# Kernel tuning notes

Measured on AMD Instinct MI355X. Metric: run time of the kernel, lower is better.

The kernel has to match this reference:

```python
import jax, jax.numpy as jnp
import numpy as np

SEQ_LEN = 4096
DIM_HALF = 2048  # x last dim = 2 * DIM_HALF
DIM_OUT = 1024
LN_EPS = 1e-5


def setup_inputs() -> dict:
    key = jax.random.key(0)
    k1, k2, k3 = jax.random.split(key, 3)
    x = jax.random.normal(k1, (SEQ_LEN, 2 * DIM_HALF), dtype=jnp.float32)
    ln_scale = jnp.ones((DIM_HALF,), dtype=jnp.float32)
    # original init is uniform(-eps/n, eps/n); scale randn similarly small
    spatial_weights = jax.random.normal(k2, (SEQ_LEN, SEQ_LEN), dtype=jnp.float32) * (0.001 / SEQ_LEN)
    spatial_biases = jnp.ones((SEQ_LEN, 1), dtype=jnp.float32)
    proj_w = jax.random.normal(k3, (DIM_HALF, DIM_OUT), dtype=jnp.float32) * (1.0 / np.sqrt(DIM_HALF))
    proj_b = jnp.zeros((DIM_OUT,), dtype=jnp.float32)
    return {"x": x, "ln_scale": ln_scale, "spatial_weights": spatial_weights,
            "spatial_biases": spatial_biases, "proj_w": proj_w, "proj_b": proj_b}


def reference(x, ln_scale, spatial_weights, spatial_biases, proj_w, proj_b):
    # split into value half and gate half
    xh, gate = jnp.split(x, 2, axis=-1)  # each (n, d)
    # LayerNorm (scale only, no offset), haiku default eps=1e-5
    mean = jnp.mean(gate, axis=-1, keepdims=True)
    var = jnp.var(gate, axis=-1, keepdims=True)
    gate = (gate - mean) * jax.lax.rsqrt(var + LN_EPS) * ln_scale
    # causal (lower-triangular) masked spatial mixing: out[m,d] = sum_n w[m,n] * gate[n,d]
    n = spatial_weights.shape[0]
    w = jnp.tril(spatial_weights)
    gate = jnp.einsum('nd,mn->md', gate, w) + spatial_biases  # (n, d)
    # gating multiply + output projection
    out = (xh * gate) @ proj_w + proj_b  # (n, dim_out)
    return out
```

## Files before the change

kernel.cpp:

```cpp
#include <hip/hip_runtime.h>
#include <cstdint>
#include <cstddef>

#define SEQ 4096
#define DH 2048
#define DOUT 1024

typedef float f32x4 __attribute__((ext_vector_type(4)));
typedef __bf16 bf16x8 __attribute__((ext_vector_type(8)));


__device__ __forceinline__ unsigned short f2bf(float f) {
  unsigned int u = __float_as_uint(f);
  unsigned int r = (u + 0x7FFFu + ((u >> 16) & 1u)) >> 16;
  return (unsigned short)r;
}

__device__ __forceinline__ void g2l16(const unsigned short* g, unsigned short* l) {
  __builtin_amdgcn_global_load_lds((__attribute__((address_space(1))) void*)(void*)g,
                                   (__attribute__((address_space(3))) void*)l, 16, 0, 0);
}


__global__ __launch_bounds__(256) void ln_stats(const float* __restrict__ x,
                                                float* __restrict__ mv,
                                                float* __restrict__ rv) {
  int row = blockIdx.x;
  const float4* g4 = (const float4*)(x + (size_t)row * (2 * DH) + DH);
  float4 a = g4[threadIdx.x];
  float4 b = g4[threadIdx.x + 256];
  float s  = a.x + a.y + a.z + a.w + b.x + b.y + b.z + b.w;
  float s2 = a.x * a.x + a.y * a.y + a.z * a.z + a.w * a.w +
             b.x * b.x + b.y * b.y + b.z * b.z + b.w * b.w;
#pragma unroll
  for (int o = 32; o > 0; o >>= 1) {
    s  += __shfl_down(s, o);
    s2 += __shfl_down(s2, o);
  }
  __shared__ float red[8];
  int wave = threadIdx.x >> 6;
  if ((threadIdx.x & 63) == 0) { red[wave] = s; red[wave + 4] = s2; }
  __syncthreads();
  if (threadIdx.x == 0) {
    float S  = red[0] + red[1] + red[2] + red[3];
    float S2 = red[4] + red[5] + red[6] + red[7];
    float mean = S * (1.0f / DH);
    float var  = S2 * (1.0f / DH) - mean * mean;
    mv[row] = mean;
    rv[row] = rsqrtf(var + 1e-5f);
  }
}


__global__ __launch_bounds__(256) void norm_tr(const float* __restrict__ x,
                                               const float* __restrict__ mv,
                                               const float* __restrict__ rv,
                                               const float* __restrict__ lns,
                                               unsigned short* __restrict__ gateT) {
  __shared__ float tile[64][65];
  int d0 = blockIdx.x * 64;
  int n0 = blockIdx.y * 64;
#pragma unroll
  for (int i = 0; i < 16; i++) {
    int idx = threadIdx.x + i * 256;
    int r = idx >> 6, c = idx & 63;
    float v = x[(size_t)(n0 + r) * (2 * DH) + DH + d0 + c];
    tile[r][c] = (v - mv[n0 + r]) * rv[n0 + r];
  }
  __syncthreads();
#pragma unroll
  for (int i = 0; i < 16; i++) {
    int idx = threadIdx.x + i * 256;
    int dr = idx >> 6, nc = idx & 63;
    float v = tile[nc][dr] * lns[d0 + dr];
    gateT[(size_t)(d0 + dr) * SEQ + n0 + nc] = f2bf(v);
  }
}


__global__ __launch_bounds__(256) void cast_w_tril(const float* __restrict__ w,
                                                   unsigned short* __restrict__ wb) {
  size_t e = ((size_t)blockIdx.x * 256 + threadIdx.x) * 8;
  int m = (int)(e >> 12);
  int k = (int)(e & 4095);
  uint4 o;
  if (k + 7 <= m) {
    const float4* s = (const float4*)(w + e);
    float4 a = s[0], b = s[1];
    o.x = (unsigned)f2bf(a.x) | ((unsigned)f2bf(a.y) << 16);
    o.y = (unsigned)f2bf(a.z) | ((unsigned)f2bf(a.w) << 16);
    o.z = (unsigned)f2bf(b.x) | ((unsigned)f2bf(b.y) << 16);
    o.w = (unsigned)f2bf(b.z) | ((unsigned)f2bf(b.w) << 16);
  } else if (k > m) {
    o.x = o.y = o.z = o.w = 0u;
  } else {
    unsigned short t[8];
#pragma unroll
    for (int j = 0; j < 8; j++) t[j] = (k + j <= m) ? f2bf(w[e + j]) : (unsigned short)0;
    o.x = (unsigned)t[0] | ((unsigned)t[1] << 16);
    o.y = (unsigned)t[2] | ((unsigned)t[3] << 16);
    o.z = (unsigned)t[4] | ((unsigned)t[5] << 16);
    o.w = (unsigned)t[6] | ((unsigned)t[7] << 16);
  }
  *(uint4*)(wb + e) = o;
}


__global__ __launch_bounds__(256) void proj_tr(const float* __restrict__ pw,
                                               unsigned short* __restrict__ pT) {
  __shared__ float tile[64][65];
  int j0 = blockIdx.x * 64;
  int d0 = blockIdx.y * 64;
#pragma unroll
  for (int i = 0; i < 16; i++) {
    int idx = threadIdx.x + i * 256;
    int r = idx >> 6, c = idx & 63;
    tile[r][c] = pw[(size_t)(d0 + r) * DOUT + j0 + c];
  }
  __syncthreads();
#pragma unroll
  for (int i = 0; i < 16; i++) {
    int idx = threadIdx.x + i * 256;
    int jr = idx >> 6, dc = idx & 63;
    pT[(size_t)(j0 + jr) * DH + d0 + dc] = f2bf(tile[dc][jr]);
  }
}


template <int BM, int BN, int EPI, bool CAUSAL>
__global__ __launch_bounds__(256) void gemm_t(const unsigned short* __restrict__ A,
                                              const unsigned short* __restrict__ BT,
                                              const float* __restrict__ xfull,
                                              const float* __restrict__ rbias,
                                              unsigned short* __restrict__ Pout,
                                              const float* __restrict__ cbias,
                                              float* __restrict__ out,
                                              int N, int K) {
  constexpr int BK = 64;
  constexpr int MI = BM / 32;
  constexpr int NJ = BN / 32;
  constexpr int ARPT = (BM * BK) / (256 * 8);
  constexpr int BRPT = (BN * BK) / (256 * 8);

  __shared__ unsigned short sA[BM * BK];
  __shared__ unsigned short sB[BN * BK];

  const int tid = threadIdx.x;
  const int lane = tid & 63, wave = tid >> 6;
  const int quad = lane >> 4, l16 = lane & 15;
  const int wm = wave >> 1, wn = wave & 1;
  const int bn0 = blockIdx.x * BN;

  int by = blockIdx.y;
  if (CAUSAL) {
    int q = by >> 4, r = by & 15;
    by = (q == 0) ? r : (q == 1) ? (31 - r) : (q == 2) ? (32 + r) : (63 - r);
  }
  const int bm0 = by * BM;
  const int kEnd = CAUSAL ? (bm0 + BM) : K;

  const unsigned short* aSrc[ARPT];
  unsigned short* aDst[ARPT];
  const unsigned short* bSrc[BRPT];
  unsigned short* bDst[BRPT];
#pragma unroll
  for (int r = 0; r < ARPT; r++) {
    int idx = r * 256 + tid;
    int row = idx >> 3;
    int col = ((idx & 7) ^ (row & 7)) * 8;
    aSrc[r] = A + (size_t)(bm0 + row) * K + col;
    aDst[r] = &sA[(size_t)idx * 8];
  }
#pragma unroll
  for (int r = 0; r < BRPT; r++) {
    int idx = r * 256 + tid;
    int row = idx >> 3;
    int col = ((idx & 7) ^ (row & 7)) * 8;
    bSrc[r] = BT + (size_t)(bn0 + row) * K + col;
    bDst[r] = &sB[(size_t)idx * 8];
  }

  f32x4 acc[MI][NJ] = {};

  for (int k0 = 0; k0 < kEnd; k0 += BK) {
#pragma unroll
    for (int r = 0; r < ARPT; r++) { g2l16(aSrc[r], aDst[r]); aSrc[r] += BK; }
#pragma unroll
    for (int r = 0; r < BRPT; r++) { g2l16(bSrc[r], bDst[r]); bSrc[r] += BK; }
    __syncthreads();

    bf16x8 af[2][MI], bfr[2][NJ];
#pragma unroll
    for (int h = 0; h < 2; h++) {
#pragma unroll
      for (int i = 0; i < MI; i++) {
        int R = wm * (BM / 2) + i * 16 + l16;
        af[h][i] = *(const bf16x8*)&sA[R * BK + (((h * 4 + quad) ^ (R & 7)) * 8)];
      }
#pragma unroll
      for (int j = 0; j < NJ; j++) {
        int R = wn * (BN / 2) + j * 16 + l16;
        bfr[h][j] = *(const bf16x8*)&sB[R * BK + (((h * 4 + quad) ^ (R & 7)) * 8)];
      }
    }
#pragma unroll
    for (int h = 0; h < 2; h++)
#pragma unroll
      for (int i = 0; i < MI; i++)
#pragma unroll
        for (int j = 0; j < NJ; j++)
          acc[i][j] = __builtin_amdgcn_mfma_f32_16x16x32_bf16(af[h][i], bfr[h][j], acc[i][j], 0, 0, 0);
    __syncthreads();
  }

#pragma unroll
  for (int i = 0; i < MI; i++) {
#pragma unroll
    for (int j = 0; j < NJ; j++) {
      int col = bn0 + wn * (BN / 2) + j * 16 + l16;
#pragma unroll
      for (int r = 0; r < 4; r++) {
        int row = bm0 + wm * (BM / 2) + i * 16 + quad * 4 + r;
        float v = acc[i][j][r];
        if (EPI == 1) {
          float g = v + rbias[row];
          float pv = xfull[(size_t)row * (2 * DH) + col] * g;
          Pout[(size_t)row * N + col] = f2bf(pv);
        } else {
          out[(size_t)row * N + col] = v + cbias[col];
        }
      }
    }
  }
}


extern "C" void kernel_launch(void* const* d_in, const int* in_sizes, int n_in,
                              void* d_out, int out_size, void* d_ws, size_t ws_size,
                              hipStream_t stream) {
  (void)in_sizes; (void)n_in; (void)out_size; (void)ws_size;
  const float* x   = (const float*)d_in[0];
  const float* lns = (const float*)d_in[1];
  const float* w   = (const float*)d_in[2];
  const float* sb  = (const float*)d_in[3];
  const float* pw  = (const float*)d_in[4];
  const float* pb  = (const float*)d_in[5];
  float* out = (float*)d_out;

  char* p = (char*)d_ws;
  unsigned short* gateT = (unsigned short*)p; p += (size_t)DH * SEQ * 2;
  unsigned short* wb    = (unsigned short*)p; p += (size_t)SEQ * SEQ * 2;
  unsigned short* projT = (unsigned short*)p; p += (size_t)DOUT * DH * 2;
  unsigned short* Pbuf  = (unsigned short*)p; p += (size_t)SEQ * DH * 2;
  float* mv = (float*)p; p += (size_t)SEQ * 4;
  float* rv = (float*)p; p += (size_t)SEQ * 4;

  ln_stats<<<SEQ, 256, 0, stream>>>(x, mv, rv);
  norm_tr<<<dim3(DH / 64, SEQ / 64), 256, 0, stream>>>(x, mv, rv, lns, gateT);
  cast_w_tril<<<(int)(((size_t)SEQ * SEQ / 8) / 256), 256, 0, stream>>>(w, wb);
  proj_tr<<<dim3(DOUT / 64, DH / 64), 256, 0, stream>>>(pw, projT);

  gemm_t<64, 128, 1, true><<<dim3(DH / 128, SEQ / 64), 256, 0, stream>>>(
      wb, gateT, x, sb, Pbuf, nullptr, nullptr, DH, SEQ);
  gemm_t<64, 64, 2, false><<<dim3(DOUT / 64, SEQ / 64), 256, 0, stream>>>(
      Pbuf, projT, nullptr, nullptr, nullptr, pb, out, DOUT, DH);
}
```

Baseline: 267.1 us.

## Double-buffer LDS in GEMMs and pair causal row tiles for load balance

Rewrites the GEMM kernel to double-buffer its LDS tiles, issuing the global-to-LDS loads for the next K tile before computing the current one. This is meant to hide load latency and drops one barrier per iteration. The causal GEMM now gives each block a pair of row tiles (i and its mirror), so every block does the same amount of triangular work, replacing the old remapped block order. Tile shapes change to 128x64 for both GEMMs. LDS use doubles, which may lower occupancy, and the causal grid halves, giving fewer but longer blocks.

```diff
diff --git a/kernel.cpp b/kernel.cpp
--- a/kernel.cpp
+++ b/kernel.cpp
@@ -127,23 +127,24 @@
 }
 
 
-template <int BM, int BN, int EPI, bool CAUSAL>
-__global__ __launch_bounds__(256) void gemm_t(const unsigned short* __restrict__ A,
-                                              const unsigned short* __restrict__ BT,
-                                              const float* __restrict__ xfull,
-                                              const float* __restrict__ rbias,
-                                              unsigned short* __restrict__ Pout,
-                                              const float* __restrict__ cbias,
-                                              float* __restrict__ out,
-                                              int N, int K) {
+template <int BM, int BN, int EPI, bool PAIR>
+__global__ __launch_bounds__(256) void gemm_db(const unsigned short* __restrict__ A,
+                                               const unsigned short* __restrict__ BT,
+                                               const float* __restrict__ xfull,
+                                               const float* __restrict__ rbias,
+                                               unsigned short* __restrict__ Pout,
+                                               const float* __restrict__ cbias,
+                                               float* __restrict__ out,
+                                               int N, int K) {
   constexpr int BK = 64;
   constexpr int MI = BM / 32;
   constexpr int NJ = BN / 32;
   constexpr int ARPT = (BM * BK) / (256 * 8);
   constexpr int BRPT = (BN * BK) / (256 * 8);
-
-  __shared__ unsigned short sA[BM * BK];
-  __shared__ unsigned short sB[BN * BK];
+  constexpr int ASZ = BM * BK, BSZ = BN * BK;
+
+  __shared__ unsigned short sA[2 * ASZ];
+  __shared__ unsigned short sB[2 * BSZ];
 
   const int tid = threadIdx.x;
   const int lane = tid & 63, wave = tid >> 6;
@@ -151,83 +152,101 @@
   const int wm = wave >> 1, wn = wave & 1;
   const int bn0 = blockIdx.x * BN;
 
-  int by = blockIdx.y;
-  if (CAUSAL) {
-    int q = by >> 4, r = by & 15;
-    by = (q == 0) ? r : (q == 1) ? (31 - r) : (q == 2) ? (32 + r) : (63 - r);
-  }
-  const int bm0 = by * BM;
-  const int kEnd = CAUSAL ? (bm0 + BM) : K;
-
-  const unsigned short* aSrc[ARPT];
-  unsigned short* aDst[ARPT];
-  const unsigned short* bSrc[BRPT];
-  unsigned short* bDst[BRPT];
-#pragma unroll
-  for (int r = 0; r < ARPT; r++) {
-    int idx = r * 256 + tid;
-    int row = idx >> 3;
-    int col = ((idx & 7) ^ (row & 7)) * 8;
-    aSrc[r] = A + (size_t)(bm0 + row) * K + col;
-    aDst[r] = &sA[(size_t)idx * 8];
-  }
-#pragma unroll
-  for (int r = 0; r < BRPT; r++) {
-    int idx = r * 256 + tid;
-    int row = idx >> 3;
-    int col = ((idx & 7) ^ (row & 7)) * 8;
-    bSrc[r] = BT + (size_t)(bn0 + row) * K + col;
-    bDst[r] = &sB[(size_t)idx * 8];
-  }
-
-  f32x4 acc[MI][NJ] = {};
-
-  for (int k0 = 0; k0 < kEnd; k0 += BK) {
-#pragma unroll
-    for (int r = 0; r < ARPT; r++) { g2l16(aSrc[r], aDst[r]); aSrc[r] += BK; }
-#pragma unroll
-    for (int r = 0; r < BRPT; r++) { g2l16(bSrc[r], bDst[r]); bSrc[r] += BK; }
+  const int nPass = PAIR ? 2 : 1;
+  for (int pass = 0; pass < nPass; pass++) {
+    const int by = PAIR ? (pass == 0 ? (int)blockIdx.y
+                                     : (2 * (int)gridDim.y - 1 - (int)blockIdx.y))
+                        : (int)blockIdx.y;
+    const int bm0 = by * BM;
+    const int nt = (PAIR ? (bm0 + BM) : K) / BK;
+
+    const unsigned short* aP[ARPT];
+    const unsigned short* bP[BRPT];
+#pragma unroll
+    for (int r = 0; r < ARPT; r++) {
+      int idx = r * 256 + tid;
+      int row = idx >> 3;
+      int col = ((idx & 7) ^ (row & 7)) * 8;
+      aP[r] = A + (size_t)(bm0 + row) * K + col;
+    }
+#pragma unroll
+    for (int r = 0; r < BRPT; r++) {
+      int idx = r * 256 + tid;
+      int row = idx >> 3;
+      int col = ((idx & 7) ^ (row & 7)) * 8;
+      bP[r] = BT + (size_t)(bn0 + row) * K + col;
+    }
+
+    f32x4 acc[MI][NJ] = {};
+
+    auto stage = [&](int buf) {
+#pragma unroll
+      for (int r = 0; r < ARPT; r++) {
+        g2l16(aP[r], &sA[buf * ASZ + (r * 256 + tid) * 8]);
+        aP[r] += BK;
+      }
+#pragma unroll
+      for (int r = 0; r < BRPT; r++) {
+        g2l16(bP[r], &sB[buf * BSZ + (r * 256 + tid) * 8]);
+        bP[r] += BK;
+      }
+    };
+
+    auto compute = [&](int buf) {
+      const unsigned short* bA = &sA[buf * ASZ];
+      const unsigned short* bB = &sB[buf * BSZ];
+      bf16x8 af[2][MI], bfr[2][NJ];
+#pragma unroll
+      for (int h = 0; h < 2; h++) {
+#pragma unroll
+        for (int i = 0; i < MI; i++) {
+          int R = wm * (BM / 2) + i * 16 + l16;
+          af[h][i] = *(const bf16x8*)&bA[R * BK + (((h * 4 + quad) ^ (R & 7)) * 8)];
+        }
+#pragma unroll
+        for (int j = 0; j < NJ; j++) {
+          int R = wn * (BN / 2) + j * 16 + l16;
+          bfr[h][j] = *(const bf16x8*)&bB[R * BK + (((h * 4 + quad) ^ (R & 7)) * 8)];
+        }
+      }
+#pragma unroll
+      for (int h = 0; h < 2; h++)
+#pragma unroll
+        for (int i = 0; i < MI; i++)
+#pragma unroll
+          for (int j = 0; j < NJ; j++)
+            acc[i][j] = __builtin_amdgcn_mfma_f32_16x16x32_bf16(af[h][i], bfr[h][j], acc[i][j], 0, 0, 0);
+    };
+
+    if (pass) __syncthreads();
+    stage(0);
     __syncthreads();
 
-    bf16x8 af[2][MI], bfr[2][NJ];
-#pragma unroll
-    for (int h = 0; h < 2; h++) {
-#pragma unroll
-      for (int i = 0; i < MI; i++) {
-        int R = wm * (BM / 2) + i * 16 + l16;
-        af[h][i] = *(const bf16x8*)&sA[R * BK + (((h * 4 + quad) ^ (R & 7)) * 8)];
-      }
+    int cur = 0;
+    for (int t = 0; t < nt - 1; t++) {
+      stage(cur ^ 1);
+      compute(cur);
+      __syncthreads();
+      cur ^= 1;
+    }
+    compute(cur);
+
+#pragma unroll
+    for (int i = 0; i < MI; i++) {
 #pragma unroll
       for (int j = 0; j < NJ; j++) {
-        int R = wn * (BN / 2) + j * 16 + l16;
-        bfr[h][j] = *(const bf16x8*)&sB[R * BK + (((h * 4 + quad) ^ (R & 7)) * 8)];
-      }
-    }
-#pragma unroll
-    for (int h = 0; h < 2; h++)
-#pragma unroll
-      for (int i = 0; i < MI; i++)
-#pragma unroll
-        for (int j = 0; j < NJ; j++)
-          acc[i][j] = __builtin_amdgcn_mfma_f32_16x16x32_bf16(af[h][i], bfr[h][j], acc[i][j], 0, 0, 0);
-    __syncthreads();
-  }
-
-#pragma unroll
-  for (int i = 0; i < MI; i++) {
-#pragma unroll
-    for (int j = 0; j < NJ; j++) {
-      int col = bn0 + wn * (BN / 2) + j * 16 + l16;
-#pragma unroll
-      for (int r = 0; r < 4; r++) {
-        int row = bm0 + wm * (BM / 2) + i * 16 + quad * 4 + r;
-        float v = acc[i][j][r];
-        if (EPI == 1) {
-          float g = v + rbias[row];
-          float pv = xfull[(size_t)row * (2 * DH) + col] * g;
-          Pout[(size_t)row * N + col] = f2bf(pv);
-        } else {
-          out[(size_t)row * N + col] = v + cbias[col];
+        int col = bn0 + wn * (BN / 2) + j * 16 + l16;
+#pragma unroll
+        for (int r = 0; r < 4; r++) {
+          int row = bm0 + wm * (BM / 2) + i * 16 + quad * 4 + r;
+          float v = acc[i][j][r];
+          if (EPI == 1) {
+            float g = v + rbias[row];
+            float pv = xfull[(size_t)row * (2 * DH) + col] * g;
+            Pout[(size_t)row * N + col] = f2bf(pv);
+          } else {
+            out[(size_t)row * N + col] = v + cbias[col];
+          }
         }
       }
     }
@@ -260,8 +279,8 @@
   cast_w_tril<<<(int)(((size_t)SEQ * SEQ / 8) / 256), 256, 0, stream>>>(w, wb);
   proj_tr<<<dim3(DOUT / 64, DH / 64), 256, 0, stream>>>(pw, projT);
 
-  gemm_t<64, 128, 1, true><<<dim3(DH / 128, SEQ / 64), 256, 0, stream>>>(
+  gemm_db<128, 64, 1, true><<<dim3(DH / 64, SEQ / 256), 256, 0, stream>>>(
       wb, gateT, x, sb, Pbuf, nullptr, nullptr, DH, SEQ);
-  gemm_t<64, 64, 2, false><<<dim3(DOUT / 64, SEQ / 64), 256, 0, stream>>>(
+  gemm_db<128, 64, 2, false><<<dim3(DOUT / 64, SEQ / 128), 256, 0, stream>>>(
       Pbuf, projT, nullptr, nullptr, nullptr, pb, out, DOUT, DH);
 }
```

After: 268.7 us. No clear change (+0.6%).
